# Kernel tuning notes

Hardware: AMD Instinct MI355X
Metric: run time of the kernel (lower is better)

## Reference

```python
import jax, jax.numpy as jnp
import numpy as np

B, T, D = 4, 2048, 1024
H, HD = 16, 64  # num_heads, head_size; H*HD == D
DFF = 4 * D
EPS = 1e-5

def _ln(x, g, b):
    mu = jnp.mean(x, axis=-1, keepdims=True)
    var = jnp.mean(jnp.square(x - mu), axis=-1, keepdims=True)
    return (x - mu) * jax.lax.rsqrt(var + EPS) * g + b

def setup_inputs() -> dict:
    key = jax.random.key(0)
    ks = jax.random.split(key, 12)
    s = lambda fan_in: 1.0 / np.sqrt(fan_in)
    return {
        "x": jax.random.normal(ks[0], (B, T, D), jnp.float32),
        "Wq": jax.random.normal(ks[1], (H, D, HD), jnp.float32) * s(D),
        "Wk": jax.random.normal(ks[2], (H, D, HD), jnp.float32) * s(D),
        "Wv": jax.random.normal(ks[3], (H, D, HD), jnp.float32) * s(D),
        "Wo": jax.random.normal(ks[4], (D, D), jnp.float32) * s(D),
        "bo": jax.random.normal(ks[5], (D,), jnp.float32) * 0.01,
        "W1": jax.random.normal(ks[6], (D, DFF), jnp.float32) * s(D),
        "b1": jax.random.normal(ks[7], (DFF,), jnp.float32) * 0.01,
        "W2": jax.random.normal(ks[8], (DFF, D), jnp.float32) * s(DFF),
        "b2": jax.random.normal(ks[9], (D,), jnp.float32) * 0.01,
        "g1": jnp.ones((D,), jnp.float32),
        "be1": jnp.zeros((D,), jnp.float32),
        "g2": jnp.ones((D,), jnp.float32),
        "be2": jnp.zeros((D,), jnp.float32),
    }

def reference(x, Wq, Wk, Wv, Wo, bo, W1, b1, W2, b2, g1, be1, g2, be2):
    # pre-LN attention
    h = _ln(x, g1, be1)                                   # [B,T,D]
    q = jnp.einsum('btd,hde->bhte', h, Wq)                # [B,H,T,HD]
    k = jnp.einsum('btd,hde->bhte', h, Wk)
    v = jnp.einsum('btd,hde->bhte', h, Wv)
    scores = jnp.einsum('bhte,bhse->bhts', q, k) * (HD ** -0.5)  # [B,H,T,T]
    mask = jnp.tril(jnp.ones((T, T), bool))
    scores = jnp.where(mask, scores, -jnp.inf)
    attn = jax.nn.softmax(scores, axis=-1)
    ctx = jnp.einsum('bhts,bhse->bhte', attn, v)          # [B,H,T,HD]
    ctx = ctx.transpose(0, 2, 1, 3).reshape(B, T, D)      # concat heads
    x = x + jnp.einsum('btd,de->bte', ctx, Wo) + bo
    # pre-LN FFN
    h2 = _ln(x, g2, be2)
    ff = jax.nn.relu(jnp.einsum('btd,df->btf', h2, W1) + b1)
    x = x + jnp.einsum('btf,fd->btd', ff, W2) + b2
    return x
```

## Files before the change

kernel.cpp:

```cpp
#include <hip/hip_runtime.h>
#include <stdint.h>

#define B_ 4
#define T_ 2048
#define D_ 1024
#define H_ 16
#define HD_ 64
#define DFF_ 4096
#define M_ (B_ * T_)

typedef __bf16 bf16x8 __attribute__((ext_vector_type(8)));
typedef float f32x4 __attribute__((ext_vector_type(4)));

__device__ __forceinline__ uint16_t f2bf(float f) {
  union { float f; uint32_t u; } v;
  v.f = f;
  uint32_t r = v.u + 0x7FFF + ((v.u >> 16) & 1);
  return (uint16_t)(r >> 16);
}

#define GLD_LDS(gp, lp)                                                        \
  __builtin_amdgcn_global_load_lds(                                            \
      (const __attribute__((address_space(1))) void*)(gp),                     \
      (__attribute__((address_space(3))) void*)(lp), 16, 0, 0)

__global__ __launch_bounds__(256) void ln_bf16(const float* __restrict__ x,
                                               const float* __restrict__ gamma,
                                               const float* __restrict__ beta,
                                               uint16_t* __restrict__ out) {
  __shared__ float red[4];
  const int tid = threadIdx.x;
  const size_t row = blockIdx.x;
  const float4 v = ((const float4*)(x + row * D_))[tid];
  float s = v.x + v.y + v.z + v.w;
#pragma unroll
  for (int off = 32; off >= 1; off >>= 1) s += __shfl_xor(s, off, 64);
  if ((tid & 63) == 0) red[tid >> 6] = s;
  __syncthreads();
  const float mean = (red[0] + red[1] + red[2] + red[3]) * (1.0f / D_);
  const float d0 = v.x - mean, d1 = v.y - mean, d2 = v.z - mean, d3 = v.w - mean;
  float ss = d0 * d0 + d1 * d1 + d2 * d2 + d3 * d3;
#pragma unroll
  for (int off = 32; off >= 1; off >>= 1) ss += __shfl_xor(ss, off, 64);
  __syncthreads();
  if ((tid & 63) == 0) red[tid >> 6] = ss;
  __syncthreads();
  const float var = (red[0] + red[1] + red[2] + red[3]) * (1.0f / D_);
  const float rstd = rsqrtf(var + 1e-5f);
  const float4 g = ((const float4*)gamma)[tid];
  const float4 b = ((const float4*)beta)[tid];
  ushort4 o;
  o.x = f2bf(d0 * rstd * g.x + b.x);
  o.y = f2bf(d1 * rstd * g.y + b.y);
  o.z = f2bf(d2 * rstd * g.z + b.z);
  o.w = f2bf(d3 * rstd * g.w + b.w);
  ((ushort4*)(out + row * D_))[tid] = o;
}

__global__ __launch_bounds__(256) void transpose_cast(const float* __restrict__ in,
                                                      uint16_t* __restrict__ out,
                                                      int R, int C) {
  __shared__ float tile[32][33];
  const int tx = threadIdx.x & 31, ty = threadIdx.x >> 5;
  const int c0 = blockIdx.x * 32, r0 = blockIdx.y * 32;
#pragma unroll
  for (int i = 0; i < 32; i += 8)
    tile[ty + i][tx] = in[(size_t)(r0 + ty + i) * C + c0 + tx];
  __syncthreads();
#pragma unroll
  for (int i = 0; i < 32; i += 8)
    out[(size_t)(c0 + ty + i) * R + r0 + tx] = f2bf(tile[tx][ty + i]);
}

__global__ __launch_bounds__(256) void qkv_wt(const float* __restrict__ Wq,
                                              const float* __restrict__ Wk,
                                              const float* __restrict__ Wv,
                                              uint16_t* __restrict__ out) {
  __shared__ float tile[32][33];
  const int tx = threadIdx.x & 31, ty = threadIdx.x >> 5;
  const int z = blockIdx.z, which = z >> 4, hh = z & 15;
  const float* W = (which == 0) ? Wq : ((which == 1) ? Wk : Wv);
  const float* in = W + (size_t)hh * D_ * HD_;
  const int e0 = blockIdx.x * 32, d0 = blockIdx.y * 32;
#pragma unroll
  for (int i = 0; i < 32; i += 8)
    tile[ty + i][tx] = in[(size_t)(d0 + ty + i) * HD_ + e0 + tx];
  __syncthreads();
#pragma unroll
  for (int i = 0; i < 32; i += 8)
    out[((size_t)(which * 1024 + hh * 64) + e0 + ty + i) * D_ + d0 + tx] =
        f2bf(tile[tx][ty + i]);
}

__global__ __launch_bounds__(256) void gemm_bf16(const uint16_t* __restrict__ A,
                                                 const uint16_t* __restrict__ Bt,
                                                 void* __restrict__ C,
                                                 const float* __restrict__ bias,
                                                 const float* __restrict__ resid,
                                                 int M, int N, int K, int lda,
                                                 int ldb, int flags) {
  __shared__ __align__(16) uint16_t As[128 * 64];
  __shared__ __align__(16) uint16_t Bs[128 * 64];
  const int tid = threadIdx.x;
  const int lane = tid & 63, w = tid >> 6;
  const int quad = lane >> 4, lr = lane & 15;
  const int wr = w >> 1, wc = w & 1;

  const int n_tiles = N >> 7;
  const int pid = blockIdx.x;
  const int grp = 16 * n_tiles;
  const int gid = pid / grp;
  const int rem = pid - gid * grp;
  const int nt = rem / 16;
  const int mt = gid * 16 + (rem - nt * 16);
  const int bn0 = nt * 128, bm0 = mt * 128;

  f32x4 acc[4][4];
#pragma unroll
  for (int i = 0; i < 4; i++)
#pragma unroll
    for (int j = 0; j < 4; j++) acc[i][j] = f32x4{0.f, 0.f, 0.f, 0.f};

  const int s_row = lane >> 3, s_slot = lane & 7;

  for (int k0 = 0; k0 < K; k0 += 64) {
#pragma unroll
    for (int u = 0; u < 4; u++) {
      const int r = w * 32 + u * 8 + s_row;
      const int cg = s_slot ^ (r & 7);
      GLD_LDS(A + (size_t)(bm0 + r) * lda + k0 + cg * 8, As + (w * 32 + u * 8) * 64);
      GLD_LDS(Bt + (size_t)(bn0 + r) * ldb + k0 + cg * 8, Bs + (w * 32 + u * 8) * 64);
    }
    __syncthreads();

#pragma unroll
    for (int ks = 0; ks < 2; ks++) {
      bf16x8 af[4], bfr[4];
#pragma unroll
      for (int i = 0; i < 4; i++) {
        const int m = wr * 64 + i * 16 + lr;
        const int slot = (ks * 4 + quad) ^ (m & 7);
        af[i] = *(const bf16x8*)(As + m * 64 + slot * 8);
      }
#pragma unroll
      for (int j = 0; j < 4; j++) {
        const int n = wc * 64 + j * 16 + lr;
        const int slot = (ks * 4 + quad) ^ (n & 7);
        bfr[j] = *(const bf16x8*)(Bs + n * 64 + slot * 8);
      }
#pragma unroll
      for (int i = 0; i < 4; i++)
#pragma unroll
        for (int j = 0; j < 4; j++)
          acc[i][j] =
              __builtin_amdgcn_mfma_f32_16x16x32_bf16(af[i], bfr[j], acc[i][j], 0, 0, 0);
    }
    __syncthreads();
  }

  const int base_m = bm0 + wr * 64 + quad * 4;
  const int base_n = bn0 + wc * 64 + lr;
#pragma unroll
  for (int i = 0; i < 4; i++) {
#pragma unroll
    for (int j = 0; j < 4; j++) {
      const int col = base_n + j * 16;
      const float bv = bias ? bias[col] : 0.f;
#pragma unroll
      for (int r = 0; r < 4; r++) {
        const size_t row = base_m + i * 16 + r;
        float v = acc[i][j][r] + bv;
        if (resid) v += resid[row * N + col];
        if (flags & 1) v = fmaxf(v, 0.f);
        if (flags & 2)
          ((uint16_t*)C)[row * N + col] = f2bf(v);
        else
          ((float*)C)[row * N + col] = v;
      }
    }
  }
}

__global__ __launch_bounds__(256) void v_transpose(const uint16_t* __restrict__ qkv,
                                                   uint16_t* __restrict__ vtb) {
  __shared__ __align__(16) uint16_t tile[64 * 72];
  const int tid = threadIdx.x;
  const int t0 = blockIdx.x * 64;
  const int bh = blockIdx.y;
  const int b = bh >> 4, h = bh & 15;
  const uint16_t* src = qkv + (size_t)b * T_ * 3072 + 2048 + h * 64;
#pragma unroll
  for (int u = 0; u < 2; u++) {
    const int uu = tid + u * 256;
    const int r = uu >> 3, c = uu & 7;
    *(int4*)(tile + r * 72 + c * 8) =
        *(const int4*)(src + (size_t)(t0 + r) * 3072 + c * 8);
  }
  __syncthreads();
  uint16_t* dst = vtb + ((size_t)bh * 64) * T_ + t0;
#pragma unroll
  for (int u = 0; u < 2; u++) {
    const int uu = tid + u * 256;
    const int e = uu >> 3, c2 = uu & 7;
    union { uint16_t u16[8]; int4 v; } tmp;
#pragma unroll
    for (int jj = 0; jj < 8; jj++) tmp.u16[jj] = tile[(c2 * 8 + jj) * 72 + e];
    *(int4*)(dst + (size_t)e * T_ + c2 * 8) = tmp.v;
  }
}

__global__ __launch_bounds__(256) void attn_mfma(const uint16_t* __restrict__ qkv,
                                                 const uint16_t* __restrict__ vtb,
                                                 uint16_t* __restrict__ ctx) {
  __shared__ __align__(16) uint16_t Ks[64 * 72];
  __shared__ __align__(16) uint16_t Vt[64 * 72];
  __shared__ __align__(16) uint16_t Ps[128 * 72];
  const int tid = threadIdx.x;
  const int lane = tid & 63, w = tid >> 6;
  const int quad = lane >> 4, lr = lane & 15;
  const int h = blockIdx.y, b = blockIdx.z;
  const uint16_t* base = qkv + (size_t)b * T_ * 3072 + h * 64;
  const uint16_t* vbase = vtb + ((size_t)(b * H_ + h) * 64) * T_;
  const int sr = tid >> 3, sc = tid & 7;

#pragma unroll
  for (int half = 0; half < 2; half++) {
    const int tq = (half == 0) ? (int)blockIdx.x : 15 - (int)blockIdx.x;
    const int q0 = tq * 128;

    bf16x8 aq[2][2];
#pragma unroll
    for (int i = 0; i < 2; i++)
#pragma unroll
      for (int ks = 0; ks < 2; ks++)
        aq[i][ks] = *(const bf16x8*)(base + (size_t)(q0 + w * 32 + i * 16 + lr) * 3072 +
                                     ks * 32 + quad * 8);

    f32x4 oacc[2][4];
#pragma unroll
    for (int i = 0; i < 2; i++)
#pragma unroll
      for (int j = 0; j < 4; j++) oacc[i][j] = f32x4{0.f, 0.f, 0.f, 0.f};
    float l_part[2] = {0.f, 0.f};

    const int row_min_w = q0 + w * 32;
    const int row_max_w = row_min_w + 31;
    const int nt = 2 * tq + 2;

    for (int st = 0; st < nt; st++) {
      __syncthreads();
#pragma unroll
      for (int u = 0; u < 2; u++) {
        const int r = sr + u * 32;
        *(int4*)(Ks + r * 72 + sc * 8) =
            *(const int4*)(base + 1024 + (size_t)(st * 64 + r) * 3072 + sc * 8);
        *(int4*)(Vt + r * 72 + sc * 8) =
            *(const int4*)(vbase + (size_t)r * T_ + st * 64 + sc * 8);
      }
      __syncthreads();

      if (st * 64 > row_max_w) continue;

      f32x4 sa[2][4];
#pragma unroll
      for (int i = 0; i < 2; i++)
#pragma unroll
        for (int sf = 0; sf < 4; sf++) sa[i][sf] = f32x4{0.f, 0.f, 0.f, 0.f};
#pragma unroll
      for (int ks = 0; ks < 2; ks++) {
        bf16x8 ak[4];
#pragma unroll
        for (int sf = 0; sf < 4; sf++)
          ak[sf] = *(const bf16x8*)(Ks + (sf * 16 + lr) * 72 + ks * 32 + quad * 8);
#pragma unroll
        for (int i = 0; i < 2; i++)
#pragma unroll
          for (int sf = 0; sf < 4; sf++)
            sa[i][sf] = __builtin_amdgcn_mfma_f32_16x16x32_bf16(ak[sf], aq[i][ks],
                                                                sa[i][sf], 0, 0, 0);
      }

#pragma unroll
      for (int i = 0; i < 2; i++) {
        const int mrow = q0 + w * 32 + i * 16 + lr;
#pragma unroll
        for (int sf = 0; sf < 4; sf++) {
          const int s0 = st * 64 + sf * 16 + quad * 4;
          float p[4];
#pragma unroll
          for (int r = 0; r < 4; r++) {
            float sv = sa[i][sf][r];
            if (s0 + r > mrow) sv = -1e30f;
            p[r] = exp2f(fmaf(sv, 0.18033688f, -28.8539008f));
            l_part[i] += p[r];
          }
          ushort4 pk;
          pk.x = f2bf(p[0]);
          pk.y = f2bf(p[1]);
          pk.z = f2bf(p[2]);
          pk.w = f2bf(p[3]);
          *(ushort4*)(Ps + (size_t)(w * 32 + i * 16 + lr) * 72 + sf * 16 + quad * 4) = pk;
        }
      }

#pragma unroll
      for (int ks = 0; ks < 2; ks++) {
        bf16x8 ap[2], bv[4];
#pragma unroll
        for (int i = 0; i < 2; i++)
          ap[i] = *(const bf16x8*)(Ps + (size_t)(w * 32 + i * 16 + lr) * 72 + ks * 32 +
                                   quad * 8);
#pragma unroll
        for (int j = 0; j < 4; j++)
          bv[j] = *(const bf16x8*)(Vt + (j * 16 + lr) * 72 + ks * 32 + quad * 8);
#pragma unroll
        for (int i = 0; i < 2; i++)
#pragma unroll
          for (int j = 0; j < 4; j++)
            oacc[i][j] =
                __builtin_amdgcn_mfma_f32_16x16x32_bf16(ap[i], bv[j], oacc[i][j], 0, 0, 0);
      }
    }

    float linv[2];
#pragma unroll
    for (int i = 0; i < 2; i++) {
      float l = l_part[i];
      l += __shfl_xor(l, 16, 64);
      l += __shfl_xor(l, 32, 64);
      linv[i] = 1.f / l;
    }
    uint16_t* ob =
        ctx + ((size_t)b * T_ + q0 + w * 32 + quad * 4) * D_ + h * 64 + lr;
#pragma unroll
    for (int i = 0; i < 2; i++)
#pragma unroll
      for (int r = 0; r < 4; r++) {
        const float inv = __shfl(linv[i], quad * 4 + r, 64);
#pragma unroll
        for (int j = 0; j < 4; j++)
          ob[(size_t)(i * 16 + r) * D_ + j * 16] = f2bf(oacc[i][j][r] * inv);
      }
  }
}

extern "C" void kernel_launch(void* const* d_in, const int* in_sizes, int n_in,
                              void* d_out, int out_size, void* d_ws, size_t ws_size,
                              hipStream_t stream) {
  const float* x = (const float*)d_in[0];
  const float* Wq = (const float*)d_in[1];
  const float* Wk = (const float*)d_in[2];
  const float* Wv = (const float*)d_in[3];
  const float* Wo = (const float*)d_in[4];
  const float* bo = (const float*)d_in[5];
  const float* W1 = (const float*)d_in[6];
  const float* b1 = (const float*)d_in[7];
  const float* W2 = (const float*)d_in[8];
  const float* b2 = (const float*)d_in[9];
  const float* g1 = (const float*)d_in[10];
  const float* be1 = (const float*)d_in[11];
  const float* g2 = (const float*)d_in[12];
  const float* be2 = (const float*)d_in[13];
  float* out = (float*)d_out;

  const size_t MB = 1024ull * 1024ull;
  if (ws_size < 200 * MB) return;
  char* ws = (char*)d_ws;
  uint16_t* hbuf = (uint16_t*)(ws + 0 * MB);
  uint16_t* wqkvt = (uint16_t*)(ws + 16 * MB);
  uint16_t* wot = (uint16_t*)(ws + 22 * MB);
  uint16_t* w1t = (uint16_t*)(ws + 24 * MB);
  uint16_t* w2t = (uint16_t*)(ws + 32 * MB);
  float* x1 = (float*)(ws + 40 * MB);
  uint16_t* qkvb = (uint16_t*)(ws + 72 * MB);
  uint16_t* ctxb = (uint16_t*)(ws + 120 * MB);
  uint16_t* vtb = (uint16_t*)(ws + 136 * MB);
  uint16_t* ffb = (uint16_t*)(ws + 136 * MB);

  qkv_wt<<<dim3(2, 32, 48), 256, 0, stream>>>(Wq, Wk, Wv, wqkvt);
  transpose_cast<<<dim3(32, 32), 256, 0, stream>>>(Wo, wot, 1024, 1024);
  transpose_cast<<<dim3(128, 32), 256, 0, stream>>>(W1, w1t, 1024, 4096);
  transpose_cast<<<dim3(32, 128), 256, 0, stream>>>(W2, w2t, 4096, 1024);

  ln_bf16<<<M_, 256, 0, stream>>>(x, g1, be1, hbuf);
  gemm_bf16<<<64 * 24, 256, 0, stream>>>(hbuf, wqkvt, qkvb, nullptr, nullptr, M_,
                                         3 * D_, D_, D_, D_, 2);
  v_transpose<<<dim3(T_ / 64, B_ * H_), 256, 0, stream>>>(qkvb, vtb);
  attn_mfma<<<dim3(8, H_, B_), 256, 0, stream>>>(qkvb, vtb, ctxb);
  gemm_bf16<<<64 * 8, 256, 0, stream>>>(ctxb, wot, x1, bo, x, M_, D_, D_, D_, D_, 0);
  ln_bf16<<<M_, 256, 0, stream>>>(x1, g2, be2, hbuf);
  gemm_bf16<<<64 * 32, 256, 0, stream>>>(hbuf, w1t, ffb, b1, nullptr, M_, DFF_, D_,
                                         D_, D_, 1 | 2);
  gemm_bf16<<<64 * 8, 256, 0, stream>>>(ffb, w2t, out, b2, x1, M_, D_, DFF_, DFF_,
                                        DFF_, 0);
}
```

Baseline: 568.1 us.

## Template GEMM tile width, use LDS-direct swizzled loads and unmasked tiles in attention

The GEMM kernel is templated on tile width so the two N=1024 GEMMs (output projection and FFN down) use 128x64 tiles. This doubles their block count from 512 to 1024 to fill more compute units. Attention now loads K and V tiles with global_load_lds into an XOR-swizzled, unpadded LDS layout instead of going through registers. It also skips the causal mask comparison on tiles that lie fully below the diagonal. Narrower tiles lower per-block data reuse, and the swizzle must match on both the write and read sides.

```diff
diff --git a/kernel.cpp b/kernel.cpp
--- a/kernel.cpp
+++ b/kernel.cpp
@@ -92,6 +92,7 @@
         f2bf(tile[tx][ty + i]);
 }
 
+template <int BN>
 __global__ __launch_bounds__(256) void gemm_bf16(const uint16_t* __restrict__ A,
                                                  const uint16_t* __restrict__ Bt,
                                                  void* __restrict__ C,
@@ -99,27 +100,28 @@
                                                  const float* __restrict__ resid,
                                                  int M, int N, int K, int lda,
                                                  int ldb, int flags) {
+  constexpr int NJ = BN / 32;
   __shared__ __align__(16) uint16_t As[128 * 64];
-  __shared__ __align__(16) uint16_t Bs[128 * 64];
+  __shared__ __align__(16) uint16_t Bs[BN * 64];
   const int tid = threadIdx.x;
   const int lane = tid & 63, w = tid >> 6;
   const int quad = lane >> 4, lr = lane & 15;
   const int wr = w >> 1, wc = w & 1;
 
-  const int n_tiles = N >> 7;
+  const int n_tiles = N / BN;
   const int pid = blockIdx.x;
   const int grp = 16 * n_tiles;
   const int gid = pid / grp;
   const int rem = pid - gid * grp;
   const int nt = rem / 16;
   const int mt = gid * 16 + (rem - nt * 16);
-  const int bn0 = nt * 128, bm0 = mt * 128;
-
-  f32x4 acc[4][4];
+  const int bn0 = nt * BN, bm0 = mt * 128;
+
+  f32x4 acc[4][NJ];
 #pragma unroll
   for (int i = 0; i < 4; i++)
 #pragma unroll
-    for (int j = 0; j < 4; j++) acc[i][j] = f32x4{0.f, 0.f, 0.f, 0.f};
+    for (int j = 0; j < NJ; j++) acc[i][j] = f32x4{0.f, 0.f, 0.f, 0.f};
 
   const int s_row = lane >> 3, s_slot = lane & 7;
 
@@ -129,13 +131,19 @@
       const int r = w * 32 + u * 8 + s_row;
       const int cg = s_slot ^ (r & 7);
       GLD_LDS(A + (size_t)(bm0 + r) * lda + k0 + cg * 8, As + (w * 32 + u * 8) * 64);
-      GLD_LDS(Bt + (size_t)(bn0 + r) * ldb + k0 + cg * 8, Bs + (w * 32 + u * 8) * 64);
+    }
+#pragma unroll
+    for (int u = 0; u < NJ; u++) {
+      const int r = w * (BN / 4) + u * 8 + s_row;
+      const int cg = s_slot ^ (r & 7);
+      GLD_LDS(Bt + (size_t)(bn0 + r) * ldb + k0 + cg * 8,
+              Bs + (w * (BN / 4) + u * 8) * 64);
     }
     __syncthreads();
 
 #pragma unroll
     for (int ks = 0; ks < 2; ks++) {
-      bf16x8 af[4], bfr[4];
+      bf16x8 af[4], bfr[NJ];
 #pragma unroll
       for (int i = 0; i < 4; i++) {
         const int m = wr * 64 + i * 16 + lr;
@@ -143,15 +151,15 @@
         af[i] = *(const bf16x8*)(As + m * 64 + slot * 8);
       }
 #pragma unroll
-      for (int j = 0; j < 4; j++) {
-        const int n = wc * 64 + j * 16 + lr;
+      for (int j = 0; j < NJ; j++) {
+        const int n = wc * (BN / 2) + j * 16 + lr;
         const int slot = (ks * 4 + quad) ^ (n & 7);
         bfr[j] = *(const bf16x8*)(Bs + n * 64 + slot * 8);
       }
 #pragma unroll
       for (int i = 0; i < 4; i++)
 #pragma unroll
-        for (int j = 0; j < 4; j++)
+        for (int j = 0; j < NJ; j++)
           acc[i][j] =
               __builtin_amdgcn_mfma_f32_16x16x32_bf16(af[i], bfr[j], acc[i][j], 0, 0, 0);
     }
@@ -159,11 +167,11 @@
   }
 
   const int base_m = bm0 + wr * 64 + quad * 4;
-  const int base_n = bn0 + wc * 64 + lr;
+  const int base_n = bn0 + wc * (BN / 2) + lr;
 #pragma unroll
   for (int i = 0; i < 4; i++) {
 #pragma unroll
-    for (int j = 0; j < 4; j++) {
+    for (int j = 0; j < NJ; j++) {
       const int col = base_n + j * 16;
       const float bv = bias ? bias[col] : 0.f;
 #pragma unroll
@@ -212,16 +220,17 @@
 __global__ __launch_bounds__(256) void attn_mfma(const uint16_t* __restrict__ qkv,
                                                  const uint16_t* __restrict__ vtb,
                                                  uint16_t* __restrict__ ctx) {
-  __shared__ __align__(16) uint16_t Ks[64 * 72];
-  __shared__ __align__(16) uint16_t Vt[64 * 72];
+  __shared__ __align__(16) uint16_t Ks[64 * 64];
+  __shared__ __align__(16) uint16_t Vt[64 * 64];
   __shared__ __align__(16) uint16_t Ps[128 * 72];
   const int tid = threadIdx.x;
   const int lane = tid & 63, w = tid >> 6;
   const int quad = lane >> 4, lr = lane & 15;
+  const int lr7 = lr & 7;
   const int h = blockIdx.y, b = blockIdx.z;
   const uint16_t* base = qkv + (size_t)b * T_ * 3072 + h * 64;
   const uint16_t* vbase = vtb + ((size_t)(b * H_ + h) * 64) * T_;
-  const int sr = tid >> 3, sc = tid & 7;
+  const int s_row = lane >> 3, s_slot = lane & 7;
 
 #pragma unroll
   for (int half = 0; half < 2; half++) {
@@ -245,17 +254,17 @@
 
     const int row_min_w = q0 + w * 32;
     const int row_max_w = row_min_w + 31;
-    const int nt = 2 * tq + 2;
-
-    for (int st = 0; st < nt; st++) {
+    const int nstg = 2 * tq + 2;
+
+    for (int st = 0; st < nstg; st++) {
       __syncthreads();
 #pragma unroll
       for (int u = 0; u < 2; u++) {
-        const int r = sr + u * 32;
-        *(int4*)(Ks + r * 72 + sc * 8) =
-            *(const int4*)(base + 1024 + (size_t)(st * 64 + r) * 3072 + sc * 8);
-        *(int4*)(Vt + r * 72 + sc * 8) =
-            *(const int4*)(vbase + (size_t)r * T_ + st * 64 + sc * 8);
+        const int r = w * 16 + u * 8 + s_row;
+        const int cg = s_slot ^ (r & 7);
+        GLD_LDS(base + 1024 + (size_t)(st * 64 + r) * 3072 + cg * 8,
+                Ks + (w * 16 + u * 8) * 64);
+        GLD_LDS(vbase + (size_t)r * T_ + st * 64 + cg * 8, Vt + (w * 16 + u * 8) * 64);
       }
       __syncthreads();
 
@@ -270,8 +279,10 @@
       for (int ks = 0; ks < 2; ks++) {
         bf16x8 ak[4];
 #pragma unroll
-        for (int sf = 0; sf < 4; sf++)
-          ak[sf] = *(const bf16x8*)(Ks + (sf * 16 + lr) * 72 + ks * 32 + quad * 8);
+        for (int sf = 0; sf < 4; sf++) {
+          const int slot = (ks * 4 + quad) ^ lr7;
+          ak[sf] = *(const bf16x8*)(Ks + (sf * 16 + lr) * 64 + slot * 8);
+        }
 #pragma unroll
         for (int i = 0; i < 2; i++)
 #pragma unroll
@@ -280,26 +291,50 @@
                                                                 sa[i][sf], 0, 0, 0);
       }
 
-#pragma unroll
-      for (int i = 0; i < 2; i++) {
-        const int mrow = q0 + w * 32 + i * 16 + lr;
-#pragma unroll
-        for (int sf = 0; sf < 4; sf++) {
-          const int s0 = st * 64 + sf * 16 + quad * 4;
-          float p[4];
-#pragma unroll
-          for (int r = 0; r < 4; r++) {
-            float sv = sa[i][sf][r];
-            if (s0 + r > mrow) sv = -1e30f;
-            p[r] = exp2f(fmaf(sv, 0.18033688f, -28.8539008f));
-            l_part[i] += p[r];
+      const bool diag = (st * 64 + 63 > row_min_w);
+      if (diag) {
+#pragma unroll
+        for (int i = 0; i < 2; i++) {
+          const int mrow = q0 + w * 32 + i * 16 + lr;
+#pragma unroll
+          for (int sf = 0; sf < 4; sf++) {
+            const int s0 = st * 64 + sf * 16 + quad * 4;
+            float p[4];
+#pragma unroll
+            for (int r = 0; r < 4; r++) {
+              float sv = sa[i][sf][r];
+              if (s0 + r > mrow) sv = -1e30f;
+              p[r] = exp2f(fmaf(sv, 0.18033688f, -28.8539008f));
+              l_part[i] += p[r];
+            }
+            ushort4 pk;
+            pk.x = f2bf(p[0]);
+            pk.y = f2bf(p[1]);
+            pk.z = f2bf(p[2]);
+            pk.w = f2bf(p[3]);
+            *(ushort4*)(Ps + (size_t)(w * 32 + i * 16 + lr) * 72 + sf * 16 + quad * 4) =
+                pk;
           }
-          ushort4 pk;
-          pk.x = f2bf(p[0]);
-          pk.y = f2bf(p[1]);
-          pk.z = f2bf(p[2]);
-          pk.w = f2bf(p[3]);
-          *(ushort4*)(Ps + (size_t)(w * 32 + i * 16 + lr) * 72 + sf * 16 + quad * 4) = pk;
+        }
+      } else {
+#pragma unroll
+        for (int i = 0; i < 2; i++) {
+#pragma unroll
+          for (int sf = 0; sf < 4; sf++) {
+            float p[4];
+#pragma unroll
+            for (int r = 0; r < 4; r++) {
+              p[r] = exp2f(fmaf(sa[i][sf][r], 0.18033688f, -28.8539008f));
+              l_part[i] += p[r];
+            }
+            ushort4 pk;
+            pk.x = f2bf(p[0]);
+            pk.y = f2bf(p[1]);
+            pk.z = f2bf(p[2]);
+            pk.w = f2bf(p[3]);
+            *(ushort4*)(Ps + (size_t)(w * 32 + i * 16 + lr) * 72 + sf * 16 + quad * 4) =
+                pk;
+          }
         }
       }
 
@@ -311,8 +346,10 @@
           ap[i] = *(const bf16x8*)(Ps + (size_t)(w * 32 + i * 16 + lr) * 72 + ks * 32 +
                                    quad * 8);
 #pragma unroll
-        for (int j = 0; j < 4; j++)
-          bv[j] = *(const bf16x8*)(Vt + (j * 16 + lr) * 72 + ks * 32 + quad * 8);
+        for (int j = 0; j < 4; j++) {
+          const int slot = (ks * 4 + quad) ^ lr7;
+          bv[j] = *(const bf16x8*)(Vt + (j * 16 + lr) * 64 + slot * 8);
+        }
 #pragma unroll
         for (int i = 0; i < 2; i++)
 #pragma unroll
@@ -383,14 +420,15 @@
   transpose_cast<<<dim3(32, 128), 256, 0, stream>>>(W2, w2t, 4096, 1024);
 
   ln_bf16<<<M_, 256, 0, stream>>>(x, g1, be1, hbuf);
-  gemm_bf16<<<64 * 24, 256, 0, stream>>>(hbuf, wqkvt, qkvb, nullptr, nullptr, M_,
-                                         3 * D_, D_, D_, D_, 2);
+  gemm_bf16<128><<<64 * 24, 256, 0, stream>>>(hbuf, wqkvt, qkvb, nullptr, nullptr,
+                                              M_, 3 * D_, D_, D_, D_, 2);
   v_transpose<<<dim3(T_ / 64, B_ * H_), 256, 0, stream>>>(qkvb, vtb);
   attn_mfma<<<dim3(8, H_, B_), 256, 0, stream>>>(qkvb, vtb, ctxb);
-  gemm_bf16<<<64 * 8, 256, 0, stream>>>(ctxb, wot, x1, bo, x, M_, D_, D_, D_, D_, 0);
+  gemm_bf16<64><<<64 * 16, 256, 0, stream>>>(ctxb, wot, x1, bo, x, M_, D_, D_, D_,
+                                             D_, 0);
   ln_bf16<<<M_, 256, 0, stream>>>(x1, g2, be2, hbuf);
-  gemm_bf16<<<64 * 32, 256, 0, stream>>>(hbuf, w1t, ffb, b1, nullptr, M_, DFF_, D_,
-                                         D_, D_, 1 | 2);
-  gemm_bf16<<<64 * 8, 256, 0, stream>>>(ffb, w2t, out, b2, x1, M_, D_, DFF_, DFF_,
-                                        DFF_, 0);
-}
+  gemm_bf16<128><<<64 * 32, 256, 0, stream>>>(hbuf, w1t, ffb, b1, nullptr, M_, DFF_,
+                                              D_, D_, D_, 1 | 2);
+  gemm_bf16<64><<<64 * 16, 256, 0, stream>>>(ffb, w2t, out, b2, x1, M_, D_, DFF_,
+                                             DFF_, DFF_, 0);
+}
```

Result: faster. 553.8 us (-2.5%).
